# Kernel tuning notes

Hardware: AMD Instinct MI355X
Metric: run time of the kernel (lower is better)

Reference implementation:

```python
import jax, jax.numpy as jnp
import numpy as np


def setup_inputs() -> dict:
    key = jax.random.key(0)
    inputs = jax.random.normal(key, (4096, 8192), dtype=jnp.float32)
    return {"inputs": inputs, "k": 512}


def reference(inputs, k):
    # Original: kth_smallest = sort_ascending(inputs)[..., n-1-k]
    # i.e. the (k+1)-th largest value per row. Equivalent via top_k.
    # Keep only elements STRICTLY greater than that threshold.
    thresh = jax.lax.top_k(inputs, k + 1)[0][..., -1]  # [batch]
    mask = (inputs > thresh[:, None]).astype(inputs.dtype)
    return inputs * mask
```

## Files before the change

kernel.cpp:

```cpp
#include <hip/hip_runtime.h>
#include <stdint.h>


constexpr int COLS  = 8192;
constexpr int TPB   = 256;
constexpr int EPT   = COLS / TPB;
constexpr int VPT   = EPT / 4;
constexpr int NBIN0 = 2048;
constexpr int CAP   = 2048;

__device__ __forceinline__ uint32_t map_f32(uint32_t u) {
  return (u & 0x80000000u) ? ~u : (u | 0x80000000u);
}
__device__ __forceinline__ float unmap_f32(uint32_t m) {
  return __uint_as_float((m & 0x80000000u) ? (m ^ 0x80000000u) : ~m);
}

__global__ __launch_bounds__(TPB)
void ksparse_kernel(const float* __restrict__ in, const int* __restrict__ kptr,
                    float* __restrict__ out) {
  __shared__ __align__(16) uint32_t hist[2 * NBIN0];
  __shared__ uint32_t th[3 * 128];
  __shared__ uint32_t wtot[4];
  __shared__ uint32_t s_packed;
  __shared__ uint32_t s_cnt;
  __shared__ uint32_t s_sel[3];

  const int t    = threadIdx.x;
  const int wave = t >> 6;
  const int lane = t & 63;
  const size_t rowbase = (size_t)blockIdx.x * COLS;

  const float4* inp = (const float4*)(in + rowbase);
  float4 v[VPT];
#pragma unroll
  for (int i = 0; i < VPT; ++i) v[i] = inp[t + i * TPB];

  uint4* h4 = (uint4*)hist;
#pragma unroll
  for (int i = 0; i < 4; ++i) h4[t + i * TPB] = make_uint4(0u, 0u, 0u, 0u);
  th[t] = 0u;
  if (t < 128) th[256 + t] = 0u;
  if (t == 0) { s_packed = 0u; s_cnt = 0u; }
  uint32_t kk = (uint32_t)(*kptr) + 1u;
  __syncthreads();

  uint32_t m[EPT];
  uint32_t* h = &hist[(wave >> 1) * NBIN0];
#pragma unroll
  for (int i = 0; i < VPT; ++i) {
    m[4 * i + 0] = map_f32(__float_as_uint(v[i].x));
    m[4 * i + 1] = map_f32(__float_as_uint(v[i].y));
    m[4 * i + 2] = map_f32(__float_as_uint(v[i].z));
    m[4 * i + 3] = map_f32(__float_as_uint(v[i].w));
    atomicAdd(&h[m[4 * i + 0] >> 21], 1u);
    atomicAdd(&h[m[4 * i + 1] >> 21], 1u);
    atomicAdd(&h[m[4 * i + 2] >> 21], 1u);
    atomicAdd(&h[m[4 * i + 3] >> 21], 1u);
  }
  __syncthreads();

  {
    const uint4* hv = (const uint4*)hist;
    uint4 a0 = hv[2 * t], a1 = hv[2 * t + 1];
    uint4 b0 = hv[512 + 2 * t], b1 = hv[512 + 2 * t + 1];
    uint32_t c0 = a0.x + b0.x, c1 = a0.y + b0.y, c2 = a0.z + b0.z, c3 = a0.w + b0.w;
    uint32_t c4 = a1.x + b1.x, c5 = a1.y + b1.y, c6 = a1.z + b1.z, c7 = a1.w + b1.w;
    uint32_t sl[8];
    sl[7] = c7;         sl[6] = sl[7] + c6; sl[5] = sl[6] + c5; sl[4] = sl[5] + c4;
    sl[3] = sl[4] + c3; sl[2] = sl[3] + c2; sl[1] = sl[2] + c1; sl[0] = sl[1] + c0;
    const uint32_t total = sl[0];

    uint32_t s = total;
#pragma unroll
    for (int off = 1; off < 64; off <<= 1) {
      uint32_t tmp = __shfl_down(s, off, 64);
      s += (lane + off < 64) ? tmp : 0u;
    }
    if (lane == 0) wtot[wave] = s;
    __syncthreads();

    uint32_t hi = 0;
#pragma unroll
    for (int w = 1; w < 4; ++w)
      if (w > wave) hi += wtot[w];
    const uint32_t excl = hi + (s - total);

    int best = -1;
#pragma unroll
    for (int j = 7; j >= 0; --j)
      if (best < 0 && excl + sl[j] >= kk) best = j;
    if (best >= 0) {
      const uint32_t above = excl + ((best < 7) ? sl[best + 1] : 0u);
      atomicMax(&s_packed, ((uint32_t)(t * 8 + best) << 14) | above);
    }
  }
  __syncthreads();

  const uint32_t pk = s_packed;
  const uint32_t d0 = pk >> 14;
  kk -= (pk & 0x3FFFu);

  uint32_t* cand = &hist[NBIN0];
#pragma unroll
  for (int i = 0; i < EPT; ++i) {
    if ((m[i] >> 21) == d0) {
      uint32_t idx = atomicAdd(&s_cnt, 1u);
      if (idx < CAP) cand[idx] = m[i] & 0x1FFFFFu;
    }
  }
  __syncthreads();
  const uint32_t Cc = (s_cnt < (uint32_t)CAP) ? s_cnt : (uint32_t)CAP;

  uint32_t tpref = 0;
#pragma unroll 1
  for (int j = 0; j < 3; ++j) {
    const int dsh = 14 - 7 * j;
    uint32_t* thj = &th[j * 128];
    for (uint32_t idx = t; idx < Cc; idx += TPB) {
      const uint32_t c = cand[idx];
      const bool ok = (j == 0) || ((c >> (dsh + 7)) == tpref);
      if (ok) atomicAdd(&thj[(c >> dsh) & 127u], 1u);
    }
    __syncthreads();

    if (wave == 0) {
      uint32_t a = thj[lane], b = thj[64 + lane];
      uint32_t sb = b, sa = a;
#pragma unroll
      for (int off = 1; off < 64; off <<= 1) {
        uint32_t t1 = __shfl_down(sb, off, 64);
        uint32_t t2 = __shfl_down(sa, off, 64);
        const bool inr = (lane + off < 64);
        sb += inr ? t1 : 0u;
        sa += inr ? t2 : 0u;
      }
      const uint32_t tb = __shfl(sb, 0, 64);
      sa += tb;
      const unsigned long long mb = __ballot(sb >= kk);
      uint32_t d, ab;
      if (mb) {
        const int hb = 63 - __builtin_clzll(mb);
        const uint32_t nx = __shfl(sb, (hb + 1) & 63, 64);
        d = 64 + hb;
        ab = (hb == 63) ? 0u : nx;
      } else {
        const unsigned long long ma = __ballot(sa >= kk);
        const int ha = 63 - __builtin_clzll(ma);
        const uint32_t nx = __shfl(sa, (ha + 1) & 63, 64);
        d = (uint32_t)ha;
        ab = (ha == 63) ? tb : nx;
      }
      if (lane == 0) s_sel[j] = (d << 16) | ab;
    }
    __syncthreads();

    const uint32_t sel = s_sel[j];
    tpref = (tpref << 7) | (sel >> 16);
    kk -= (sel & 0xFFFFu);
  }

  const uint32_t T = (d0 << 21) | tpref;

  float4* op = (float4*)(out + rowbase);
#pragma unroll
  for (int i = 0; i < VPT; ++i) {
    float4 w;
    uint32_t mm;
    mm = m[4 * i + 0]; w.x = (mm > T) ? unmap_f32(mm) : 0.0f;
    mm = m[4 * i + 1]; w.y = (mm > T) ? unmap_f32(mm) : 0.0f;
    mm = m[4 * i + 2]; w.z = (mm > T) ? unmap_f32(mm) : 0.0f;
    mm = m[4 * i + 3]; w.w = (mm > T) ? unmap_f32(mm) : 0.0f;
    op[t + i * TPB] = w;
  }
}

extern "C" void kernel_launch(void* const* d_in, const int* in_sizes, int n_in,
                              void* d_out, int out_size, void* d_ws, size_t ws_size,
                              hipStream_t stream) {
  const float* in  = (const float*)d_in[0];
  const int*   k   = (const int*)d_in[1];
  float*       out = (float*)d_out;
  int rows = in_sizes[0] / COLS;
  if (rows < 1) rows = 1;
  ksparse_kernel<<<rows, TPB, 0, stream>>>(in, k, out);
}
```

Baseline: 235.1 us.

## Split fused top-k masking kernel into threshold and apply kernels

Splits the single fused kernel in two. The first computes the per-row threshold via the radix histogram and writes it to workspace. The second re-reads the input and applies the strict-greater mask. This frees the 32 mapped keys per thread from having to stay live through the selection phase, which may ease register pressure and allow more occupancy. The cost is a second full read of the input, an extra kernel launch, and a float comparison in place of the mapped-integer comparison, which could treat -0.0 versus 0.0 differently.

```diff
diff --git a/kernel.cpp b/kernel.cpp
--- a/kernel.cpp
+++ b/kernel.cpp
@@ -17,8 +17,8 @@
 }
 
 __global__ __launch_bounds__(TPB)
-void ksparse_kernel(const float* __restrict__ in, const int* __restrict__ kptr,
-                    float* __restrict__ out) {
+void thresh_kernel(const float* __restrict__ in, const int* __restrict__ kptr,
+                   float* __restrict__ thr) {
   __shared__ __align__(16) uint32_t hist[2 * NBIN0];
   __shared__ uint32_t th[3 * 128];
   __shared__ uint32_t wtot[4];
@@ -160,18 +160,28 @@
     kk -= (sel & 0xFFFFu);
   }
 
-  const uint32_t T = (d0 << 21) | tpref;
+  if (t == 0) {
+    const uint32_t T = (d0 << 21) | tpref;
+    thr[blockIdx.x] = unmap_f32(T);
+  }
+}
 
+__global__ __launch_bounds__(TPB)
+void apply_kernel(const float* __restrict__ in, const float* __restrict__ thr,
+                  float* __restrict__ out) {
+  const int t = threadIdx.x;
+  const size_t rowbase = (size_t)blockIdx.x * COLS;
+  const float tv = thr[blockIdx.x];
+  const float4* ip = (const float4*)(in + rowbase);
   float4* op = (float4*)(out + rowbase);
 #pragma unroll
   for (int i = 0; i < VPT; ++i) {
-    float4 w;
-    uint32_t mm;
-    mm = m[4 * i + 0]; w.x = (mm > T) ? unmap_f32(mm) : 0.0f;
-    mm = m[4 * i + 1]; w.y = (mm > T) ? unmap_f32(mm) : 0.0f;
-    mm = m[4 * i + 2]; w.z = (mm > T) ? unmap_f32(mm) : 0.0f;
-    mm = m[4 * i + 3]; w.w = (mm > T) ? unmap_f32(mm) : 0.0f;
-    op[t + i * TPB] = w;
+    float4 v = ip[t + i * TPB];
+    v.x = (v.x > tv) ? v.x : 0.0f;
+    v.y = (v.y > tv) ? v.y : 0.0f;
+    v.z = (v.z > tv) ? v.z : 0.0f;
+    v.w = (v.w > tv) ? v.w : 0.0f;
+    op[t + i * TPB] = v;
   }
 }
 
@@ -181,7 +191,9 @@
   const float* in  = (const float*)d_in[0];
   const int*   k   = (const int*)d_in[1];
   float*       out = (float*)d_out;
+  float*       thr = (float*)d_ws;
   int rows = in_sizes[0] / COLS;
   if (rows < 1) rows = 1;
-  ksparse_kernel<<<rows, TPB, 0, stream>>>(in, k, out);
+  thresh_kernel<<<rows, TPB, 0, stream>>>(in, k, thr);
+  apply_kernel<<<rows, TPB, 0, stream>>>(in, thr, out);
 }
```

New measurement: 249.5 us. +6.1%, slower.

## Process four rows per block with next-row prefetch and single-wave refinement

Applied to the files above, without the earlier changes.

Each block now handles four rows in sequence and issues the global loads for the next row while the current row's histogram and selection run. This is meant to hide load latency behind compute. The three-level refinement of candidates is moved into wave 0 alone, using wave-local histogram clearing, which removes several block-wide barriers per row. The trade-offs are higher register pressure from holding both v and m arrays, a grid cut to a quarter of its size (1024 blocks), and serial refinement on one wave.

```diff
diff --git a/kernel.cpp b/kernel.cpp
--- a/kernel.cpp
+++ b/kernel.cpp
@@ -8,6 +8,7 @@
 constexpr int VPT   = EPT / 4;
 constexpr int NBIN0 = 2048;
 constexpr int CAP   = 2048;
+constexpr int RPB   = 4;
 
 __device__ __forceinline__ uint32_t map_f32(uint32_t u) {
   return (u & 0x80000000u) ? ~u : (u | 0x80000000u);
@@ -16,162 +17,178 @@
   return __uint_as_float((m & 0x80000000u) ? (m ^ 0x80000000u) : ~m);
 }
 
-__global__ __launch_bounds__(TPB)
+__global__ __launch_bounds__(TPB, 4)
 void ksparse_kernel(const float* __restrict__ in, const int* __restrict__ kptr,
-                    float* __restrict__ out) {
+                    float* __restrict__ out, int rows) {
   __shared__ __align__(16) uint32_t hist[2 * NBIN0];
-  __shared__ uint32_t th[3 * 128];
+  __shared__ uint32_t th[128];
   __shared__ uint32_t wtot[4];
   __shared__ uint32_t s_packed;
   __shared__ uint32_t s_cnt;
-  __shared__ uint32_t s_sel[3];
+  __shared__ uint32_t s_T;
 
   const int t    = threadIdx.x;
   const int wave = t >> 6;
   const int lane = t & 63;
-  const size_t rowbase = (size_t)blockIdx.x * COLS;
-
-  const float4* inp = (const float4*)(in + rowbase);
+  const int row0 = blockIdx.x * RPB;
+  const uint32_t krank = (uint32_t)(*kptr) + 1u;
+
+  uint4* h4 = (uint4*)hist;
+#pragma unroll
+  for (int i = 0; i < 4; ++i) h4[t + i * TPB] = make_uint4(0u, 0u, 0u, 0u);
+  if (t == 0) { s_packed = 0u; s_cnt = 0u; }
+
   float4 v[VPT];
-#pragma unroll
-  for (int i = 0; i < VPT; ++i) v[i] = inp[t + i * TPB];
-
-  uint4* h4 = (uint4*)hist;
-#pragma unroll
-  for (int i = 0; i < 4; ++i) h4[t + i * TPB] = make_uint4(0u, 0u, 0u, 0u);
-  th[t] = 0u;
-  if (t < 128) th[256 + t] = 0u;
-  if (t == 0) { s_packed = 0u; s_cnt = 0u; }
-  uint32_t kk = (uint32_t)(*kptr) + 1u;
-  __syncthreads();
-
-  uint32_t m[EPT];
-  uint32_t* h = &hist[(wave >> 1) * NBIN0];
-#pragma unroll
-  for (int i = 0; i < VPT; ++i) {
-    m[4 * i + 0] = map_f32(__float_as_uint(v[i].x));
-    m[4 * i + 1] = map_f32(__float_as_uint(v[i].y));
-    m[4 * i + 2] = map_f32(__float_as_uint(v[i].z));
-    m[4 * i + 3] = map_f32(__float_as_uint(v[i].w));
-    atomicAdd(&h[m[4 * i + 0] >> 21], 1u);
-    atomicAdd(&h[m[4 * i + 1] >> 21], 1u);
-    atomicAdd(&h[m[4 * i + 2] >> 21], 1u);
-    atomicAdd(&h[m[4 * i + 3] >> 21], 1u);
+  if (row0 < rows) {
+    const float4* inp = (const float4*)(in + (size_t)row0 * COLS);
+#pragma unroll
+    for (int i = 0; i < VPT; ++i) v[i] = inp[t + i * TPB];
   }
   __syncthreads();
 
-  {
-    const uint4* hv = (const uint4*)hist;
-    uint4 a0 = hv[2 * t], a1 = hv[2 * t + 1];
-    uint4 b0 = hv[512 + 2 * t], b1 = hv[512 + 2 * t + 1];
-    uint32_t c0 = a0.x + b0.x, c1 = a0.y + b0.y, c2 = a0.z + b0.z, c3 = a0.w + b0.w;
-    uint32_t c4 = a1.x + b1.x, c5 = a1.y + b1.y, c6 = a1.z + b1.z, c7 = a1.w + b1.w;
-    uint32_t sl[8];
-    sl[7] = c7;         sl[6] = sl[7] + c6; sl[5] = sl[6] + c5; sl[4] = sl[5] + c4;
-    sl[3] = sl[4] + c3; sl[2] = sl[3] + c2; sl[1] = sl[2] + c1; sl[0] = sl[1] + c0;
-    const uint32_t total = sl[0];
-
-    uint32_t s = total;
-#pragma unroll
-    for (int off = 1; off < 64; off <<= 1) {
-      uint32_t tmp = __shfl_down(s, off, 64);
-      s += (lane + off < 64) ? tmp : 0u;
-    }
-    if (lane == 0) wtot[wave] = s;
-    __syncthreads();
-
-    uint32_t hi = 0;
-#pragma unroll
-    for (int w = 1; w < 4; ++w)
-      if (w > wave) hi += wtot[w];
-    const uint32_t excl = hi + (s - total);
-
-    int best = -1;
-#pragma unroll
-    for (int j = 7; j >= 0; --j)
-      if (best < 0 && excl + sl[j] >= kk) best = j;
-    if (best >= 0) {
-      const uint32_t above = excl + ((best < 7) ? sl[best + 1] : 0u);
-      atomicMax(&s_packed, ((uint32_t)(t * 8 + best) << 14) | above);
-    }
-  }
-  __syncthreads();
-
-  const uint32_t pk = s_packed;
-  const uint32_t d0 = pk >> 14;
-  kk -= (pk & 0x3FFFu);
-
-  uint32_t* cand = &hist[NBIN0];
-#pragma unroll
-  for (int i = 0; i < EPT; ++i) {
-    if ((m[i] >> 21) == d0) {
-      uint32_t idx = atomicAdd(&s_cnt, 1u);
-      if (idx < CAP) cand[idx] = m[i] & 0x1FFFFFu;
-    }
-  }
-  __syncthreads();
-  const uint32_t Cc = (s_cnt < (uint32_t)CAP) ? s_cnt : (uint32_t)CAP;
-
-  uint32_t tpref = 0;
 #pragma unroll 1
-  for (int j = 0; j < 3; ++j) {
-    const int dsh = 14 - 7 * j;
-    uint32_t* thj = &th[j * 128];
-    for (uint32_t idx = t; idx < Cc; idx += TPB) {
-      const uint32_t c = cand[idx];
-      const bool ok = (j == 0) || ((c >> (dsh + 7)) == tpref);
-      if (ok) atomicAdd(&thj[(c >> dsh) & 127u], 1u);
+  for (int i = 0; i < RPB; ++i) {
+    const int r = row0 + i;
+    if (r >= rows) break;
+
+    uint32_t m[EPT];
+#pragma unroll
+    for (int j = 0; j < VPT; ++j) {
+      m[4 * j + 0] = map_f32(__float_as_uint(v[j].x));
+      m[4 * j + 1] = map_f32(__float_as_uint(v[j].y));
+      m[4 * j + 2] = map_f32(__float_as_uint(v[j].z));
+      m[4 * j + 3] = map_f32(__float_as_uint(v[j].w));
+    }
+
+    if (i + 1 < RPB && r + 1 < rows) {
+      const float4* inn = (const float4*)(in + (size_t)(r + 1) * COLS);
+#pragma unroll
+      for (int j = 0; j < VPT; ++j) v[j] = inn[t + j * TPB];
+    }
+
+    uint32_t* h = &hist[(wave >> 1) * NBIN0];
+#pragma unroll
+    for (int j = 0; j < EPT; ++j) atomicAdd(&h[m[j] >> 21], 1u);
+    __syncthreads();
+
+    uint32_t excl, sl0;
+    {
+      const uint4* hv = (const uint4*)hist;
+      uint4 a0 = hv[2 * t], a1 = hv[2 * t + 1];
+      uint4 b0 = hv[512 + 2 * t], b1 = hv[512 + 2 * t + 1];
+      uint32_t c0 = a0.x + b0.x, c1 = a0.y + b0.y, c2 = a0.z + b0.z, c3 = a0.w + b0.w;
+      uint32_t c4 = a1.x + b1.x, c5 = a1.y + b1.y, c6 = a1.z + b1.z, c7 = a1.w + b1.w;
+      uint32_t sl[8];
+      sl[7] = c7;         sl[6] = sl[7] + c6; sl[5] = sl[6] + c5; sl[4] = sl[5] + c4;
+      sl[3] = sl[4] + c3; sl[2] = sl[3] + c2; sl[1] = sl[2] + c1; sl[0] = sl[1] + c0;
+      const uint32_t total = sl[0];
+
+      uint32_t s = total;
+#pragma unroll
+      for (int off = 1; off < 64; off <<= 1) {
+        uint32_t tmp = __shfl_down(s, off, 64);
+        s += (lane + off < 64) ? tmp : 0u;
+      }
+      if (lane == 0) wtot[wave] = s;
+      __syncthreads();
+
+      uint32_t hi = 0;
+#pragma unroll
+      for (int w = 1; w < 4; ++w)
+        if (w > wave) hi += wtot[w];
+      excl = hi + (s - total);
+      sl0 = total;
+
+      int best = -1;
+#pragma unroll
+      for (int j = 7; j >= 0; --j)
+        if (best < 0 && excl + sl[j] >= krank) best = j;
+      if (best >= 0) {
+        const uint32_t above = excl + ((best < 7) ? sl[best + 1] : 0u);
+        atomicMax(&s_packed, ((uint32_t)(t * 8 + best) << 14) | above);
+      }
+    }
+    __syncthreads();
+
+    const uint32_t pk = s_packed;
+    const uint32_t d0 = pk >> 14;
+
+    uint32_t* cand = &hist[NBIN0];
+#pragma unroll
+    for (int j = 0; j < EPT; ++j) {
+      if ((m[j] >> 21) == d0) {
+        uint32_t idx = atomicAdd(&s_cnt, 1u);
+        if (idx < CAP) cand[idx] = m[j] & 0x1FFFFFu;
+      }
     }
     __syncthreads();
 
     if (wave == 0) {
-      uint32_t a = thj[lane], b = thj[64 + lane];
-      uint32_t sb = b, sa = a;
-#pragma unroll
-      for (int off = 1; off < 64; off <<= 1) {
-        uint32_t t1 = __shfl_down(sb, off, 64);
-        uint32_t t2 = __shfl_down(sa, off, 64);
-        const bool inr = (lane + off < 64);
-        sb += inr ? t1 : 0u;
-        sa += inr ? t2 : 0u;
-      }
-      const uint32_t tb = __shfl(sb, 0, 64);
-      sa += tb;
-      const unsigned long long mb = __ballot(sb >= kk);
-      uint32_t d, ab;
-      if (mb) {
-        const int hb = 63 - __builtin_clzll(mb);
-        const uint32_t nx = __shfl(sb, (hb + 1) & 63, 64);
-        d = 64 + hb;
-        ab = (hb == 63) ? 0u : nx;
-      } else {
-        const unsigned long long ma = __ballot(sa >= kk);
-        const int ha = 63 - __builtin_clzll(ma);
-        const uint32_t nx = __shfl(sa, (ha + 1) & 63, 64);
-        d = (uint32_t)ha;
-        ab = (ha == 63) ? tb : nx;
-      }
-      if (lane == 0) s_sel[j] = (d << 16) | ab;
-    }
-    __syncthreads();
-
-    const uint32_t sel = s_sel[j];
-    tpref = (tpref << 7) | (sel >> 16);
-    kk -= (sel & 0xFFFFu);
-  }
-
-  const uint32_t T = (d0 << 21) | tpref;
-
-  float4* op = (float4*)(out + rowbase);
-#pragma unroll
-  for (int i = 0; i < VPT; ++i) {
-    float4 w;
-    uint32_t mm;
-    mm = m[4 * i + 0]; w.x = (mm > T) ? unmap_f32(mm) : 0.0f;
-    mm = m[4 * i + 1]; w.y = (mm > T) ? unmap_f32(mm) : 0.0f;
-    mm = m[4 * i + 2]; w.z = (mm > T) ? unmap_f32(mm) : 0.0f;
-    mm = m[4 * i + 3]; w.w = (mm > T) ? unmap_f32(mm) : 0.0f;
-    op[t + i * TPB] = w;
+      uint32_t kk = krank - (pk & 0x3FFFu);
+      const uint32_t Cc = (s_cnt < (uint32_t)CAP) ? s_cnt : (uint32_t)CAP;
+      uint32_t tpref = 0;
+#pragma unroll 1
+      for (int j = 0; j < 3; ++j) {
+        const int dsh = 14 - 7 * j;
+        th[lane] = 0u; th[64 + lane] = 0u;
+        for (uint32_t idx = lane; idx < Cc; idx += 64) {
+          const uint32_t c = cand[idx];
+          const bool ok = (j == 0) || ((c >> (dsh + 7)) == tpref);
+          if (ok) atomicAdd(&th[(c >> dsh) & 127u], 1u);
+        }
+        uint32_t a = th[lane], b = th[64 + lane];
+        uint32_t sb = b, sa = a;
+#pragma unroll
+        for (int off = 1; off < 64; off <<= 1) {
+          uint32_t t1 = __shfl_down(sb, off, 64);
+          uint32_t t2 = __shfl_down(sa, off, 64);
+          const bool inr = (lane + off < 64);
+          sb += inr ? t1 : 0u;
+          sa += inr ? t2 : 0u;
+        }
+        const uint32_t tb = __shfl(sb, 0, 64);
+        sa += tb;
+        const unsigned long long mb = __ballot(sb >= kk);
+        uint32_t d, ab;
+        if (mb) {
+          const int hb = 63 - __builtin_clzll(mb);
+          const uint32_t nx = __shfl(sb, (hb + 1) & 63, 64);
+          d = 64 + (uint32_t)hb;
+          ab = (hb == 63) ? 0u : nx;
+        } else {
+          const unsigned long long ma = __ballot(sa >= kk);
+          const int ha = 63 - __builtin_clzll(ma);
+          const uint32_t nx = __shfl(sa, (ha + 1) & 63, 64);
+          d = (uint32_t)ha;
+          ab = (ha == 63) ? tb : nx;
+        }
+        tpref = (tpref << 7) | d;
+        kk -= ab;
+      }
+      if (lane == 0) s_T = (d0 << 21) | tpref;
+    }
+    __syncthreads();
+
+    const uint32_t T = s_T;
+
+    float4* op = (float4*)(out + (size_t)r * COLS);
+#pragma unroll
+    for (int j = 0; j < VPT; ++j) {
+      float4 w;
+      uint32_t mm;
+      mm = m[4 * j + 0]; w.x = (mm > T) ? unmap_f32(mm) : 0.0f;
+      mm = m[4 * j + 1]; w.y = (mm > T) ? unmap_f32(mm) : 0.0f;
+      mm = m[4 * j + 2]; w.z = (mm > T) ? unmap_f32(mm) : 0.0f;
+      mm = m[4 * j + 3]; w.w = (mm > T) ? unmap_f32(mm) : 0.0f;
+      op[t + j * TPB] = w;
+    }
+
+    if (i + 1 < RPB) {
+#pragma unroll
+      for (int j = 0; j < 4; ++j) h4[t + j * TPB] = make_uint4(0u, 0u, 0u, 0u);
+      if (t == 0) { s_packed = 0u; s_cnt = 0u; }
+      __syncthreads();
+    }
   }
 }
 
@@ -183,5 +200,6 @@
   float*       out = (float*)d_out;
   int rows = in_sizes[0] / COLS;
   if (rows < 1) rows = 1;
-  ksparse_kernel<<<rows, TPB, 0, stream>>>(in, k, out);
-}
+  const int grid = (rows + RPB - 1) / RPB;
+  ksparse_kernel<<<grid, TPB, 0, stream>>>(in, k, out, rows);
+}
```

Measured after the change: 259.0 us. +10.2%, slower.
